# Kernel tuning notes

Hardware: AMD Instinct MI355X
Metric: run time of the kernel (lower is better)

Reference implementation:

```python
import jax, jax.numpy as jnp
import numpy as np

NUM_RADIAL = 6
HIDDEN = 128
OUT_EMB = 256
OUT_CH = 128
NUM_LAYERS = 3
E = 1600000
N_NODES = 50000


def setup_inputs() -> dict:
    key = jax.random.key(0)
    ks = jax.random.split(key, 16)
    inp = {
        "x": jax.random.normal(ks[0], (E, HIDDEN), dtype=jnp.float32),
        "rbf": jax.random.normal(ks[1], (E, NUM_RADIAL), dtype=jnp.float32),
        "idx_i": jax.random.randint(ks[2], (E,), 0, N_NODES, dtype=jnp.int32),
        "num_nodes": N_NODES,
        # torch nn.Linear weights are [out, in]
        "W_basis": jax.random.normal(ks[3], (HIDDEN, NUM_RADIAL), dtype=jnp.float32) * 0.3,
        "W_proj": jax.random.normal(ks[4], (OUT_EMB, HIDDEN), dtype=jnp.float32) * 0.08,
        "W_final": jax.random.normal(ks[5], (OUT_CH, OUT_EMB), dtype=jnp.float32) * 0.06,
    }
    for l in range(NUM_LAYERS):
        inp[f"W{l}"] = jax.random.normal(ks[6 + 2 * l], (OUT_EMB, OUT_EMB), dtype=jnp.float32) * 0.06
        inp[f"b{l}"] = jnp.zeros((OUT_EMB,), dtype=jnp.float32)
    return inp


def reference(x, rbf, idx_i, num_nodes, W_basis, W_proj, W_final, W0, b0, W1, b1, W2, b2):
    # basis_transformation: [E, num_radial] -> [E, hidden]
    basis = rbf @ W_basis.T
    # elementwise mul then edge->node scatter-sum
    msg = basis * x                                  # [E, hidden]
    agg = jax.ops.segment_sum(msg, idx_i, num_segments=num_nodes)  # [N, hidden]
    # output_projection (no bias)
    h = agg @ W_proj.T                                # [N, out_emb]
    for W, b in ((W0, b0), (W1, b1), (W2, b2)):
        h = jax.nn.silu(h @ W.T + b)
    return h @ W_final.T                              # [N, out_channels]
```

## Files before the change

### kernel.cpp

```cpp
#include <hip/hip_runtime.h>

typedef float f4 __attribute__((ext_vector_type(4)));
typedef float f2 __attribute__((ext_vector_type(2)));
typedef int   i4 __attribute__((ext_vector_type(4)));
typedef short bf16x8 __attribute__((ext_vector_type(8)));
typedef unsigned short u16x8 __attribute__((ext_vector_type(8)));
typedef unsigned short u16x4 __attribute__((ext_vector_type(4)));
typedef float f32x4 __attribute__((ext_vector_type(4)));

constexpr int HIDDEN     = 128;
constexpr int OUT_EMB    = 256;
constexpr int OUT_CH     = 128;
constexpr int NUM_RADIAL = 6;
constexpr int NBLK       = 128;

constexpr int OFF_Wp = 0;
constexpr int OFF_W0 = OFF_Wp + 256 * 128;
constexpr int OFF_W1 = OFF_W0 + 256 * 256;
constexpr int OFF_W2 = OFF_W1 + 256 * 256;
constexpr int OFF_Wf = OFF_W2 + 256 * 256;
constexpr int WTOT   = OFF_Wf + 128 * 256;

__device__ __forceinline__ unsigned short f2bf(float f) {
    unsigned int u = __float_as_uint(f);
    return (unsigned short)((u + 0x7FFFu + ((u >> 16) & 1u)) >> 16);
}
__device__ __forceinline__ float bf2f(unsigned short h) {
    return __uint_as_float(((unsigned int)h) << 16);
}

__global__ __launch_bounds__(256) void prep_kernel(
    const float* __restrict__ Wp, const float* __restrict__ W0,
    const float* __restrict__ W1, const float* __restrict__ W2,
    const float* __restrict__ Wf,
    unsigned short* __restrict__ whi, unsigned short* __restrict__ wlo,
    int* __restrict__ count, int N)
{
    const int i = blockIdx.x * 256 + threadIdx.x;
    if (i < N) count[i] = 0;
    if (i < WTOT) {
        const float* src; int off;
        if      (i < OFF_W0) { src = Wp; off = i - OFF_Wp; }
        else if (i < OFF_W1) { src = W0; off = i - OFF_W0; }
        else if (i < OFF_W2) { src = W1; off = i - OFF_W1; }
        else if (i < OFF_Wf) { src = W2; off = i - OFF_W2; }
        else                 { src = Wf; off = i - OFF_Wf; }
        float v = src[off];
        unsigned short h = f2bf(v);
        whi[i] = h;
        wlo[i] = f2bf(v - bf2f(h));
    }
}

__global__ __launch_bounds__(256) void hist_kernel(const int* __restrict__ idx,
                                                   int* __restrict__ count, long E)
{
    long i = ((long)blockIdx.x * blockDim.x + threadIdx.x) * 4;
    if (i + 3 < E) {
        i4 v = *(const i4*)(idx + i);
#pragma unroll
        for (int k = 0; k < 4; ++k) atomicAdd(&count[v[k]], 1);
    } else {
        for (long t = i; t < E; ++t) atomicAdd(&count[idx[t]], 1);
    }
}

__global__ __launch_bounds__(256) void scan_bsum_kernel(const int* __restrict__ count,
                                                        int* __restrict__ bsum, int N)
{
    __shared__ int red[4];
    const int i = blockIdx.x * 256 + threadIdx.x;
    int v = (i < N) ? count[i] : 0;
#pragma unroll
    for (int off = 1; off < 64; off <<= 1) v += __shfl_xor(v, off);
    if ((threadIdx.x & 63) == 0) red[threadIdx.x >> 6] = v;
    __syncthreads();
    if (threadIdx.x == 0) bsum[blockIdx.x] = red[0] + red[1] + red[2] + red[3];
}

__global__ __launch_bounds__(256) void scan_base_kernel(const int* __restrict__ bsum,
                                                        int* __restrict__ bbase,
                                                        int* __restrict__ start,
                                                        int nb, int N, int E)
{
    __shared__ int s[256];
    const int t = threadIdx.x;
    int v = (t < nb) ? bsum[t] : 0;
    s[t] = v;
    __syncthreads();
    for (int off = 1; off < 256; off <<= 1) {
        int a = s[t];
        int b = (t >= off) ? s[t - off] : 0;
        __syncthreads();
        s[t] = a + b;
        __syncthreads();
    }
    if (t < nb) bbase[t] = s[t] - v;
    if (t == 0) start[N] = E;
}

__global__ __launch_bounds__(256) void scan_write_kernel(const int* __restrict__ count,
                                                         const int* __restrict__ bbase,
                                                         int* __restrict__ start,
                                                         int* __restrict__ cursor, int N)
{
    __shared__ int s[256];
    const int t = threadIdx.x;
    const int i = blockIdx.x * 256 + t;
    int v = (i < N) ? count[i] : 0;
    s[t] = v;
    __syncthreads();
    for (int off = 1; off < 256; off <<= 1) {
        int a = s[t];
        int b = (t >= off) ? s[t - off] : 0;
        __syncthreads();
        s[t] = a + b;
        __syncthreads();
    }
    if (i < N) {
        int sv = bbase[blockIdx.x] + s[t] - v;
        start[i]  = sv;
        cursor[i] = sv;
    }
}

__global__ __launch_bounds__(256) void scatter_perm_kernel(const int* __restrict__ idx,
                                                           int* __restrict__ cursor,
                                                           int* __restrict__ perm, long E)
{
    long i = ((long)blockIdx.x * blockDim.x + threadIdx.x) * 4;
    if (i + 3 < E) {
        i4 v = *(const i4*)(idx + i);
#pragma unroll
        for (int k = 0; k < 4; ++k) {
            int p = atomicAdd(&cursor[v[k]], 1);
            perm[p] = (int)(i + k);
        }
    } else {
        for (long t = i; t < E; ++t) {
            int p = atomicAdd(&cursor[idx[t]], 1);
            perm[p] = (int)t;
        }
    }
}

__device__ __forceinline__ void edge_accum(const float* __restrict__ x,
                                           const float* __restrict__ rbf,
                                           const float wb[4][NUM_RADIAL],
                                           int e, int l, f4& acc)
{
    const float* rp = rbf + (long)e * NUM_RADIAL;
    f2 r01 = *(const f2*)(rp);
    f2 r23 = *(const f2*)(rp + 2);
    f2 r45 = *(const f2*)(rp + 4);
    f4 xv  = *(const f4*)(x + (long)e * HIDDEN + 4 * l);
    float rb[NUM_RADIAL] = {r01[0], r01[1], r23[0], r23[1], r45[0], r45[1]};
#pragma unroll
    for (int c = 0; c < 4; ++c) {
        float b = 0.f;
#pragma unroll
        for (int r = 0; r < NUM_RADIAL; ++r) b = __builtin_fmaf(rb[r], wb[c][r], b);
        acc[c] = __builtin_fmaf(b, xv[c], acc[c]);
    }
}

__global__ __launch_bounds__(256, 6) void gather_kernel(
    const float* __restrict__ x, const float* __restrict__ rbf,
    const float* __restrict__ Wb, const int* __restrict__ perm,
    const int* __restrict__ start, unsigned short* __restrict__ aggb,
    int N, int nwaves)
{
    const int lane = threadIdx.x & 63;
    const int half = lane >> 5;
    const int l    = lane & 31;
    const int wgid = blockIdx.x * (blockDim.x >> 6) + (threadIdx.x >> 6);

    float wb[4][NUM_RADIAL];
#pragma unroll
    for (int c = 0; c < 4; ++c)
#pragma unroll
        for (int r = 0; r < NUM_RADIAL; ++r)
            wb[c][r] = Wb[(4 * l + c) * NUM_RADIAL + r];

    for (int node = wgid; node < N; node += nwaves) {
        const int j0 = start[node], j1 = start[node + 1];
        f4 acc = {0.f, 0.f, 0.f, 0.f};

        int j = j0 + half;
        for (; j + 6 < j1; j += 8) {
            const int e0 = perm[j];
            const int e1 = perm[j + 2];
            const int e2 = perm[j + 4];
            const int e3 = perm[j + 6];
            edge_accum(x, rbf, wb, e0, l, acc);
            edge_accum(x, rbf, wb, e1, l, acc);
            edge_accum(x, rbf, wb, e2, l, acc);
            edge_accum(x, rbf, wb, e3, l, acc);
        }
        for (; j < j1; j += 2) edge_accum(x, rbf, wb, perm[j], l, acc);

#pragma unroll
        for (int c = 0; c < 4; ++c) acc[c] += __shfl_xor(acc[c], 32);

        if (half == 0) {
            u16x4 o;
#pragma unroll
            for (int c = 0; c < 4; ++c) o[c] = f2bf(acc[c]);
            *(u16x4*)(aggb + (long)node * HIDDEN + 4 * l) = o;
        }
    }
}

__device__ __forceinline__ int swz(int node, int col) {
    return (node * 256 + col) ^ ((node & 7) << 3);
}

template <int IN, int OUT, bool BIAS_ACT, bool LAST>
__device__ __forceinline__ void mfma_layer(
    const unsigned short* __restrict__ whi, const unsigned short* __restrict__ wlo,
    const float* __restrict__ bias,
    unsigned short* H, float* __restrict__ outp,
    int node0, int N, int wm, int wn, int lane)
{
    const int lr = lane & 15;
    const int lg = lane >> 4;
    constexpr int NT = OUT / 64;
    const int wbase = wn * (OUT / 4);
    const int mrow0 = wm * 64;

    f32x4 acc[4][NT];
#pragma unroll
    for (int nt = 0; nt < NT; ++nt) {
        float bb = 0.f;
        if constexpr (BIAS_ACT) bb = bias[wbase + nt * 16 + lr];
#pragma unroll
        for (int mt = 0; mt < 4; ++mt) {
            acc[mt][nt][0] = bb; acc[mt][nt][1] = bb;
            acc[mt][nt][2] = bb; acc[mt][nt][3] = bb;
        }
    }

    for (int ks = 0; ks < IN / 32; ++ks) {
        const int k0 = ks * 32 + lg * 8;
        bf16x8 ah[4];
#pragma unroll
        for (int mt = 0; mt < 4; ++mt)
            ah[mt] = *(const bf16x8*)&H[swz(mrow0 + mt * 16 + lr, k0)];
#pragma unroll
        for (int nt = 0; nt < NT; ++nt) {
            const long wrow = (long)(wbase + nt * 16 + lr) * IN + k0;
            bf16x8 bh = *(const bf16x8*)&whi[wrow];
            bf16x8 bl = *(const bf16x8*)&wlo[wrow];
#pragma unroll
            for (int mt = 0; mt < 4; ++mt) {
                acc[mt][nt] = __builtin_amdgcn_mfma_f32_16x16x32_bf16(ah[mt], bh, acc[mt][nt], 0, 0, 0);
                acc[mt][nt] = __builtin_amdgcn_mfma_f32_16x16x32_bf16(ah[mt], bl, acc[mt][nt], 0, 0, 0);
            }
        }
    }

    __syncthreads();

#pragma unroll
    for (int mt = 0; mt < 4; ++mt) {
#pragma unroll
        for (int nt = 0; nt < NT; ++nt) {
#pragma unroll
            for (int r = 0; r < 4; ++r) {
                float v = acc[mt][nt][r];
                if constexpr (BIAS_ACT) v = v / (1.f + __expf(-v));
                const int node = mrow0 + mt * 16 + lg * 4 + r;
                const int col  = wbase + nt * 16 + lr;
                if constexpr (LAST) {
                    if (node0 + node < N) outp[(long)(node0 + node) * OUT + col] = v;
                } else {
                    H[swz(node, col)] = f2bf(v);
                }
            }
        }
    }
    if constexpr (!LAST) __syncthreads();
}

__global__ __launch_bounds__(512, 4) void node_mlp_mfma_kernel(
    const unsigned short* __restrict__ aggb,
    const unsigned short* __restrict__ whi, const unsigned short* __restrict__ wlo,
    const float* __restrict__ b0, const float* __restrict__ b1,
    const float* __restrict__ b2,
    float* __restrict__ out, int N)
{
    __shared__ unsigned short H[NBLK * 256];

    const int tid   = threadIdx.x;
    const int w     = tid >> 6;
    const int lane  = tid & 63;
    const int wm    = w >> 2;
    const int wn    = w & 3;
    const int node0 = blockIdx.x * NBLK;

#pragma unroll
    for (int i = 0; i < (NBLK * HIDDEN) / (512 * 8); ++i) {
        const int e    = (i * 512 + tid) * 8;
        const int node = e >> 7;
        const int col  = e & 127;
        u16x8 v = {0, 0, 0, 0, 0, 0, 0, 0};
        if (node0 + node < N) v = *(const u16x8*)(aggb + (long)(node0 + node) * HIDDEN + col);
        *(u16x8*)&H[swz(node, col)] = v;
    }
    __syncthreads();

    mfma_layer<HIDDEN,  OUT_EMB, false, false>(whi + OFF_Wp, wlo + OFF_Wp, nullptr, H, nullptr, node0, N, wm, wn, lane);
    mfma_layer<OUT_EMB, OUT_EMB, true,  false>(whi + OFF_W0, wlo + OFF_W0, b0,      H, nullptr, node0, N, wm, wn, lane);
    mfma_layer<OUT_EMB, OUT_EMB, true,  false>(whi + OFF_W1, wlo + OFF_W1, b1,      H, nullptr, node0, N, wm, wn, lane);
    mfma_layer<OUT_EMB, OUT_EMB, true,  false>(whi + OFF_W2, wlo + OFF_W2, b2,      H, nullptr, node0, N, wm, wn, lane);
    mfma_layer<OUT_EMB, OUT_CH,  false, true >(whi + OFF_Wf, wlo + OFF_Wf, nullptr, H, out,     node0, N, wm, wn, lane);
}

extern "C" void kernel_launch(void* const* d_in, const int* in_sizes, int n_in,
                              void* d_out, int out_size, void* d_ws, size_t ws_size,
                              hipStream_t stream)
{
    const float* x   = (const float*)d_in[0];
    const float* rbf = (const float*)d_in[1];
    const int*   idx = (const int*)d_in[2];
    const float* Wb  = (const float*)d_in[4];
    const float* Wp  = (const float*)d_in[5];
    const float* Wf  = (const float*)d_in[6];
    const float* W0  = (const float*)d_in[7];
    const float* b0  = (const float*)d_in[8];
    const float* W1  = (const float*)d_in[9];
    const float* b1  = (const float*)d_in[10];
    const float* W2  = (const float*)d_in[11];
    const float* b2  = (const float*)d_in[12];

    const long E = (long)in_sizes[0] / HIDDEN;
    const int  N = out_size / OUT_CH;
    const int  nb = (N + 255) / 256;

    unsigned short* aggb = (unsigned short*)d_ws;
    int* count  = (int*)(aggb + (long)N * HIDDEN);
    int* startp = count + N;
    int* cursor = startp + N + 1;
    int* bsum   = cursor + N;
    int* bbase  = bsum + nb;
    int* perm   = bbase + nb;
    uintptr_t p = (uintptr_t)(perm + E);
    p = (p + 15) & ~(uintptr_t)15;
    unsigned short* whi = (unsigned short*)p;
    unsigned short* wlo = whi + WTOT;

    const int pb = (max((int)WTOT, N) + 255) / 256;
    prep_kernel<<<pb, 256, 0, stream>>>(Wp, W0, W1, W2, Wf, whi, wlo, count, N);

    const long Eq = (E + 3) / 4;
    const int eb = (int)((Eq + 255) / 256);
    hist_kernel<<<eb, 256, 0, stream>>>(idx, count, E);

    scan_bsum_kernel<<<nb, 256, 0, stream>>>(count, bsum, N);
    scan_base_kernel<<<1, 256, 0, stream>>>(bsum, bbase, startp, nb, N, (int)E);
    scan_write_kernel<<<nb, 256, 0, stream>>>(count, bbase, startp, cursor, N);

    scatter_perm_kernel<<<eb, 256, 0, stream>>>(idx, cursor, perm, E);

    const int gblocks = 2048;
    const int nwaves  = gblocks * 4;
    gather_kernel<<<gblocks, 256, 0, stream>>>(x, rbf, Wb, perm, startp, aggb, N, nwaves);

    node_mlp_mfma_kernel<<<(N + NBLK - 1) / NBLK, 512, 0, stream>>>(
        aggb, whi, wlo, b0, b1, b2, (float*)d_out, N);
}
```

Baseline: 611.5 us.

## Materialize bf16 messages in sorted order and fuse segment reduction into MLP

Replaces the permutation scatter plus random-gather kernel with a kernel that streams x and rbf in edge order, computes each message, and writes it as bf16 into its CSR-sorted slot. The per-node segment sum moves into the MLP kernel's prologue, which reads contiguous message rows, so the intermediate aggregate buffer goes away. Reads of x become coalesced instead of random gathers. The cost is an extra bf16 E×128 write and read (about 400MB each way), per-edge bf16 rounding before summation, and a serial per-wave reduction inside the MLP blocks that may stall the MFMA phase.

```diff
diff --git a/kernel.cpp b/kernel.cpp
--- a/kernel.cpp
+++ b/kernel.cpp
@@ -124,56 +124,14 @@
     }
 }
 
-__global__ __launch_bounds__(256) void scatter_perm_kernel(const int* __restrict__ idx,
-                                                           int* __restrict__ cursor,
-                                                           int* __restrict__ perm, long E)
-{
-    long i = ((long)blockIdx.x * blockDim.x + threadIdx.x) * 4;
-    if (i + 3 < E) {
-        i4 v = *(const i4*)(idx + i);
-#pragma unroll
-        for (int k = 0; k < 4; ++k) {
-            int p = atomicAdd(&cursor[v[k]], 1);
-            perm[p] = (int)(i + k);
-        }
-    } else {
-        for (long t = i; t < E; ++t) {
-            int p = atomicAdd(&cursor[idx[t]], 1);
-            perm[p] = (int)t;
-        }
-    }
-}
-
-__device__ __forceinline__ void edge_accum(const float* __restrict__ x,
-                                           const float* __restrict__ rbf,
-                                           const float wb[4][NUM_RADIAL],
-                                           int e, int l, f4& acc)
-{
-    const float* rp = rbf + (long)e * NUM_RADIAL;
-    f2 r01 = *(const f2*)(rp);
-    f2 r23 = *(const f2*)(rp + 2);
-    f2 r45 = *(const f2*)(rp + 4);
-    f4 xv  = *(const f4*)(x + (long)e * HIDDEN + 4 * l);
-    float rb[NUM_RADIAL] = {r01[0], r01[1], r23[0], r23[1], r45[0], r45[1]};
-#pragma unroll
-    for (int c = 0; c < 4; ++c) {
-        float b = 0.f;
-#pragma unroll
-        for (int r = 0; r < NUM_RADIAL; ++r) b = __builtin_fmaf(rb[r], wb[c][r], b);
-        acc[c] = __builtin_fmaf(b, xv[c], acc[c]);
-    }
-}
-
-__global__ __launch_bounds__(256, 6) void gather_kernel(
+__global__ __launch_bounds__(256) void scatter_mat_kernel(
     const float* __restrict__ x, const float* __restrict__ rbf,
-    const float* __restrict__ Wb, const int* __restrict__ perm,
-    const int* __restrict__ start, unsigned short* __restrict__ aggb,
-    int N, int nwaves)
-{
-    const int lane = threadIdx.x & 63;
-    const int half = lane >> 5;
-    const int l    = lane & 31;
-    const int wgid = blockIdx.x * (blockDim.x >> 6) + (threadIdx.x >> 6);
+    const float* __restrict__ Wb, const int* __restrict__ idx,
+    int* __restrict__ cursor, unsigned short* __restrict__ msgC, long E)
+{
+    const int l    = threadIdx.x & 31;
+    const int half = (threadIdx.x >> 5) & 1;
+    const int hw   = threadIdx.x >> 5;
 
     float wb[4][NUM_RADIAL];
 #pragma unroll
@@ -182,32 +140,29 @@
         for (int r = 0; r < NUM_RADIAL; ++r)
             wb[c][r] = Wb[(4 * l + c) * NUM_RADIAL + r];
 
-    for (int node = wgid; node < N; node += nwaves) {
-        const int j0 = start[node], j1 = start[node + 1];
-        f4 acc = {0.f, 0.f, 0.f, 0.f};
-
-        int j = j0 + half;
-        for (; j + 6 < j1; j += 8) {
-            const int e0 = perm[j];
-            const int e1 = perm[j + 2];
-            const int e2 = perm[j + 4];
-            const int e3 = perm[j + 6];
-            edge_accum(x, rbf, wb, e0, l, acc);
-            edge_accum(x, rbf, wb, e1, l, acc);
-            edge_accum(x, rbf, wb, e2, l, acc);
-            edge_accum(x, rbf, wb, e3, l, acc);
-        }
-        for (; j < j1; j += 2) edge_accum(x, rbf, wb, perm[j], l, acc);
-
-#pragma unroll
-        for (int c = 0; c < 4; ++c) acc[c] += __shfl_xor(acc[c], 32);
-
-        if (half == 0) {
-            u16x4 o;
-#pragma unroll
-            for (int c = 0; c < 4; ++c) o[c] = f2bf(acc[c]);
-            *(u16x4*)(aggb + (long)node * HIDDEN + 4 * l) = o;
-        }
+    for (long e = (long)blockIdx.x * 8 + hw; e < E; e += (long)gridDim.x * 8) {
+        const int node = idx[e];
+        int pos;
+        if (l == 0) pos = atomicAdd(&cursor[node], 1);
+        pos = __shfl(pos, half << 5);
+
+        const float* rp = rbf + e * NUM_RADIAL;
+        f2 r01 = *(const f2*)(rp);
+        f2 r23 = *(const f2*)(rp + 2);
+        f2 r45 = *(const f2*)(rp + 4);
+        f4 xv  = *(const f4*)(x + e * HIDDEN + 4 * l);
+        float rr[NUM_RADIAL] = {r01[0], r01[1], r23[0], r23[1], r45[0], r45[1]};
+
+        u16x4 o;
+#pragma unroll
+        for (int c = 0; c < 4; ++c) {
+            float b = 0.f;
+#pragma unroll
+            for (int r = 0; r < NUM_RADIAL; ++r)
+                b = __builtin_fmaf(rr[r], wb[c][r], b);
+            o[c] = f2bf(b * xv[c]);
+        }
+        *(u16x4*)(msgC + (long)pos * HIDDEN + 4 * l) = o;
     }
 }
 
@@ -283,7 +238,8 @@
 }
 
 __global__ __launch_bounds__(512, 4) void node_mlp_mfma_kernel(
-    const unsigned short* __restrict__ aggb,
+    const unsigned short* __restrict__ msgC,
+    const int* __restrict__ startp,
     const unsigned short* __restrict__ whi, const unsigned short* __restrict__ wlo,
     const float* __restrict__ b0, const float* __restrict__ b1,
     const float* __restrict__ b2,
@@ -298,14 +254,37 @@
     const int wn    = w & 3;
     const int node0 = blockIdx.x * NBLK;
 
-#pragma unroll
-    for (int i = 0; i < (NBLK * HIDDEN) / (512 * 8); ++i) {
-        const int e    = (i * 512 + tid) * 8;
-        const int node = e >> 7;
-        const int col  = e & 127;
-        u16x8 v = {0, 0, 0, 0, 0, 0, 0, 0};
-        if (node0 + node < N) v = *(const u16x8*)(aggb + (long)(node0 + node) * HIDDEN + col);
-        *(u16x8*)&H[swz(node, col)] = v;
+    for (int nn = 0; nn < 16; ++nn) {
+        const int lrow = w * 16 + nn;
+        const int node = node0 + lrow;
+        float aa[16];
+#pragma unroll
+        for (int k = 0; k < 16; ++k) aa[k] = 0.f;
+
+        if (node < N) {
+            const int j0 = startp[node], j1 = startp[node + 1];
+            int j = j0;
+            for (; j + 7 < j1; j += 8) {
+                unsigned int v[8];
+#pragma unroll
+                for (int k = 0; k < 8; ++k)
+                    v[k] = *(const unsigned int*)(msgC + (long)(j + k) * HIDDEN + 2 * lane);
+#pragma unroll
+                for (int k = 0; k < 8; ++k) {
+                    aa[2 * (k & 3)]     += bf2f((unsigned short)(v[k] & 0xffff));
+                    aa[2 * (k & 3) + 1] += bf2f((unsigned short)(v[k] >> 16));
+                }
+            }
+            for (; j < j1; ++j) {
+                unsigned int v = *(const unsigned int*)(msgC + (long)j * HIDDEN + 2 * lane);
+                aa[0] += bf2f((unsigned short)(v & 0xffff));
+                aa[1] += bf2f((unsigned short)(v >> 16));
+            }
+        }
+        float s0 = (aa[0] + aa[2]) + (aa[4] + aa[6]);
+        float s1 = (aa[1] + aa[3]) + (aa[5] + aa[7]);
+        unsigned int packed = (unsigned int)f2bf(s0) | ((unsigned int)f2bf(s1) << 16);
+        *(unsigned int*)&H[swz(lrow, 2 * lane)] = packed;
     }
     __syncthreads();
 
@@ -337,17 +316,16 @@
     const int  N = out_size / OUT_CH;
     const int  nb = (N + 255) / 256;
 
-    unsigned short* aggb = (unsigned short*)d_ws;
-    int* count  = (int*)(aggb + (long)N * HIDDEN);
+    int* count  = (int*)d_ws;
     int* startp = count + N;
     int* cursor = startp + N + 1;
     int* bsum   = cursor + N;
     int* bbase  = bsum + nb;
-    int* perm   = bbase + nb;
-    uintptr_t p = (uintptr_t)(perm + E);
-    p = (p + 15) & ~(uintptr_t)15;
-    unsigned short* whi = (unsigned short*)p;
-    unsigned short* wlo = whi + WTOT;
+    uintptr_t p = (uintptr_t)(bbase + nb);
+    p = (p + 255) & ~(uintptr_t)255;
+    unsigned short* msgC = (unsigned short*)p;
+    unsigned short* whi  = msgC + (long)E * HIDDEN;
+    unsigned short* wlo  = whi + WTOT;
 
     const int pb = (max((int)WTOT, N) + 255) / 256;
     prep_kernel<<<pb, 256, 0, stream>>>(Wp, W0, W1, W2, Wf, whi, wlo, count, N);
@@ -360,12 +338,8 @@
     scan_base_kernel<<<1, 256, 0, stream>>>(bsum, bbase, startp, nb, N, (int)E);
     scan_write_kernel<<<nb, 256, 0, stream>>>(count, bbase, startp, cursor, N);
 
-    scatter_perm_kernel<<<eb, 256, 0, stream>>>(idx, cursor, perm, E);
-
-    const int gblocks = 2048;
-    const int nwaves  = gblocks * 4;
-    gather_kernel<<<gblocks, 256, 0, stream>>>(x, rbf, Wb, perm, startp, aggb, N, nwaves);
+    scatter_mat_kernel<<<8192, 256, 0, stream>>>(x, rbf, Wb, idx, cursor, msgC, E);
 
     node_mlp_mfma_kernel<<<(N + NBLK - 1) / NBLK, 512, 0, stream>>>(
-        aggb, whi, wlo, b0, b1, b2, (float*)d_out, N);
-}
+        msgC, startp, whi, wlo, b0, b1, b2, (float*)d_out, N);
+}
```

After: 654.3 us. 7.0% more time.
